# Performance work log

Measured on AMD Instinct MI355X. Metric: run time of the kernel, lower is better.

The kernel has to match this reference:

```python
import jax, jax.numpy as jnp
import numpy as np

N = 50000      # nodes
E = 800000     # edges
IN_C = 128
HID = 96
OUT_C = 40
L = 8          # num_layers
ALPHA = 0.1
THETA = 0.5
DROPOUT = 0.5


def setup_inputs() -> dict:
    key = jax.random.key(0)
    ks = jax.random.split(key, 6)
    x = jax.random.normal(ks[0], (N, IN_C), dtype=jnp.float32)
    edge_index = jax.random.randint(ks[1], (2, E), 0, N, dtype=jnp.int64)
    proj_w = jax.random.normal(ks[2], (IN_C, HID), dtype=jnp.float32) / np.sqrt(IN_C)
    proj_b = jnp.zeros((HID,), dtype=jnp.float32)
    conv_ws = jax.random.normal(ks[3], (L, HID, HID), dtype=jnp.float32) / np.sqrt(HID)
    out_w = jax.random.normal(ks[4], (2 * HID, OUT_C), dtype=jnp.float32) / np.sqrt(2 * HID)
    out_b = jnp.zeros((OUT_C,), dtype=jnp.float32)
    return {"x": x, "edge_index": edge_index, "proj_w": proj_w, "proj_b": proj_b,
            "conv_ws": conv_ws, "out_w": out_w, "out_b": out_b}


def reference(x, edge_index, proj_w, proj_b, conv_ws, out_w, out_b):
    # --- GCN normalization with self loops (computed once, as GCN2Conv caches it) ---
    loops = jnp.arange(N, dtype=edge_index.dtype)
    src = jnp.concatenate([edge_index[0], loops])   # [E+N]
    dst = jnp.concatenate([edge_index[1], loops])
    deg = jax.ops.segment_sum(jnp.ones(E + N, dtype=x.dtype), dst, num_segments=N)
    dis = jax.lax.rsqrt(deg)                        # deg >= 1 due to self loops
    norm = dis[src] * dis[dst]                      # [E+N]

    h0 = x @ proj_w + proj_b                        # [N, HID]
    h = h0
    key = jax.random.key(42)
    for k in range(L):
        delta = 1.0 / 2 ** k
        kq, ke, kd, key = jax.random.split(key, 4)
        # dithered quantization
        b = (jax.random.uniform(kq, h.shape, dtype=h.dtype) - 0.5) * delta
        h_q = jnp.floor((h + b) / delta) * delta - b
        # GCN2Conv: propagate + initial residual + identity mapping (shared weights)
        agg = jax.ops.segment_sum(h_q[src] * norm[:, None], dst, num_segments=N)
        t = (1.0 - ALPHA) * agg + ALPHA * h0
        beta = float(np.log(THETA / (k + 1) + 1.0))
        h = (1.0 - beta) * t + beta * (t @ conv_ws[k])
        # gaussian noise + relu
        h = jax.nn.relu(h + 0.01 * jax.random.normal(ke, h.shape, dtype=h.dtype))
        if k != L - 1:
            keep = 1.0 - DROPOUT
            mask = jax.random.bernoulli(kd, keep, h.shape)
            h = jnp.where(mask, h / keep, 0.0)
    return jnp.concatenate([h0, h], axis=-1) @ out_w + out_b
```

## Files before the change

### kernel.cpp

```cpp
#include <hip/hip_runtime.h>
#include <hip/hip_fp16.h>
#include <cstdint>
#include <cmath>

#define HID 96
#define INC 128
#define OUTC 40
#define ROWS 32

typedef int      v4i __attribute__((ext_vector_type(4)));
typedef float    v4f __attribute__((ext_vector_type(4)));
typedef unsigned v2u __attribute__((ext_vector_type(2)));

__device__ __forceinline__ int4 ntld_i4(const int* p){
  v4i v = __builtin_nontemporal_load((const v4i*)p);
  return make_int4(v.x, v.y, v.z, v.w);
}
__device__ __forceinline__ float4 ntld_f4(const float* p){
  v4f v = __builtin_nontemporal_load((const v4f*)p);
  return make_float4(v.x, v.y, v.z, v.w);
}
__device__ __forceinline__ void ntst_u2(void* p, unsigned lo, unsigned hi){
  v2u v; v.x = lo; v.y = hi;
  __builtin_nontemporal_store(v, (v2u*)p);
}
__device__ __forceinline__ void ntst_f4(float* p, float a, float b, float c, float d){
  v4f v; v.x = a; v.y = b; v.z = c; v.w = d;
  __builtin_nontemporal_store(v, (v4f*)p);
}

__device__ __forceinline__ unsigned rotl32d(unsigned x, int r){ return (x<<r)|(x>>(32-r)); }

__device__ __forceinline__ void tf2x32_dev(unsigned k0, unsigned k1, unsigned x0, unsigned x1,
                                           unsigned &y0, unsigned &y1){
  unsigned ks2 = k0 ^ k1 ^ 0x1BD11BDAu;
  x0 += k0; x1 += k1;
#define TFR(r) { x0 += x1; x1 = rotl32d(x1, r); x1 ^= x0; }
  TFR(13) TFR(15) TFR(26) TFR(6)   x0 += k1;  x1 += ks2 + 1u;
  TFR(17) TFR(29) TFR(16) TFR(24)  x0 += ks2; x1 += k0 + 2u;
  TFR(13) TFR(15) TFR(26) TFR(6)   x0 += k0;  x1 += k1 + 3u;
  TFR(17) TFR(29) TFR(16) TFR(24)  x0 += k1;  x1 += ks2 + 4u;
  TFR(13) TFR(15) TFR(26) TFR(6)   x0 += ks2; x1 += k0 + 5u;
#undef TFR
  y0 = x0; y1 = x1;
}

__device__ __forceinline__ unsigned tf_bits(unsigned k0, unsigned k1, unsigned idx){
  unsigned y0, y1; tf2x32_dev(k0, k1, 0u, idx, y0, y1); return y0 ^ y1;
}

__device__ __forceinline__ float u01_from_bits(unsigned bits){
  return __uint_as_float((bits >> 9) | 0x3f800000u) - 1.0f;
}

__device__ __forceinline__ float erfinv_xla(float x){
  float w = -log1pf(-x*x);
  float p;
  if (w < 5.0f){
    w = w - 2.5f;
    p = 2.81022636e-08f;
    p = fmaf(p,w, 3.43273939e-07f);
    p = fmaf(p,w,-3.5233877e-06f);
    p = fmaf(p,w,-4.39150654e-06f);
    p = fmaf(p,w, 0.00021858087f);
    p = fmaf(p,w,-0.00125372503f);
    p = fmaf(p,w,-0.00417768164f);
    p = fmaf(p,w, 0.246640727f);
    p = fmaf(p,w, 1.50140941f);
  } else {
    w = sqrtf(w) - 3.0f;
    p = -0.000200214257f;
    p = fmaf(p,w, 0.000100950558f);
    p = fmaf(p,w, 0.00134934322f);
    p = fmaf(p,w,-0.00367342844f);
    p = fmaf(p,w, 0.00573950773f);
    p = fmaf(p,w,-0.0076224613f);
    p = fmaf(p,w, 0.00943887047f);
    p = fmaf(p,w, 1.00167406f);
    p = fmaf(p,w, 2.83297682f);
  }
  return p*x;
}

__global__ void k_detect(const unsigned* __restrict__ raw, int* flag){
  unsigned v = raw[2*threadIdx.x + 1];
  unsigned long long m = __ballot(v == 0u);
  if (threadIdx.x == 0) *flag = (m == 0xFFFFFFFFFFFFFFFFull) ? 1 : 0;
}

__global__ void k_convcount(const unsigned* __restrict__ raw, const int* __restrict__ flag,
                            int E, int* __restrict__ cnt){
  int e = blockIdx.x*256 + threadIdx.x; if (e >= E) return;
  int d;
  if (*flag) d = (int)raw[2*((size_t)E + e)];
  else       d = ((const int*)raw)[E + e];
  atomicAdd(&cnt[d], 1);
}

__global__ void k_hist(const int* __restrict__ cnt, int N, int* __restrict__ bcnt){
  __shared__ int lh[64];
  int tid = threadIdx.x; int n = blockIdx.x*256 + tid;
  if (tid < 64) lh[tid] = 0;
  __syncthreads();
  if (n < N) atomicAdd(&lh[min(cnt[n], 63)], 1);
  __syncthreads();
  if (tid < 64){
    int c = lh[tid];
    if (c > 0) atomicAdd(&bcnt[tid], c);
  }
}

__global__ void k_bucketoff(int* __restrict__ bcnt){
  __shared__ int sb[64];
  int tid = threadIdx.x;
  sb[tid] = bcnt[tid];
  __syncthreads();
  int off = 0;
  for (int b2 = tid+1; b2 < 64; b2++) off += sb[b2];
  bcnt[tid] = off;
}

__global__ void k_perm(const int* __restrict__ cnt, int N, int* __restrict__ boff,
                       int* __restrict__ perm, int* __restrict__ iperm,
                       float* __restrict__ diso, float* __restrict__ dsqr,
                       int* __restrict__ degv, int* __restrict__ degp){
  __shared__ int lh[64];
  int tid = threadIdx.x; int n = blockIdx.x*256 + tid;
  int v = (n < N) ? cnt[n] : 0;
  if (tid < 64) lh[tid] = 0;
  __syncthreads();
  int b = min(v, 63), r = 0;
  if (n < N) r = atomicAdd(&lh[b], 1);
  __syncthreads();
  if (tid < 64){
    int c = lh[tid];
    lh[tid] = (c > 0) ? atomicAdd(&boff[tid], c) : 0;
  }
  __syncthreads();
  if (n < N){
    int pos = lh[b] + r;
    perm[pos] = n;
    iperm[n] = pos;
    diso[n] = 1.0f / sqrtf((float)(v + 1));
    dsqr[pos] = 1.0f / (float)(v + 1);
    degv[pos] = v;
    degp[pos] = (v + 7) & ~7;
  }
}

__global__ void k_scanA(const int* __restrict__ degp, int N, int* __restrict__ psum){
  __shared__ int sh[256];
  int tid = threadIdx.x; int n = blockIdx.x*256 + tid;
  sh[tid] = (n < N) ? degp[n] : 0;
  for (int off = 128; off > 0; off >>= 1){
    __syncthreads();
    if (tid < off) sh[tid] += sh[tid + off];
  }
  __syncthreads();
  if (tid == 0) psum[blockIdx.x] = sh[0];
}

__global__ void k_scanB(int* __restrict__ psum, int nb){
  __shared__ int sh[256];
  int tid = threadIdx.x;
  int v = (tid < nb) ? psum[tid] : 0;
  sh[tid] = v;
  __syncthreads();
  for (int off = 1; off < 256; off <<= 1){
    int t = (tid >= off) ? sh[tid - off] : 0;
    __syncthreads();
    sh[tid] += t;
    __syncthreads();
  }
  if (tid < nb) psum[tid] = sh[tid] - v;
}

__global__ void k_rowptr2(const int* __restrict__ degv, const int* __restrict__ degp,
                          const int* __restrict__ psum, int N,
                          int* __restrict__ rowptr, int* __restrict__ csr_src,
                          float* __restrict__ csr_w){
  __shared__ int sh[256];
  int tid = threadIdx.x; int n = blockIdx.x*256 + tid;
  int vp = (n < N) ? degp[n] : 0;
  sh[tid] = vp;
  __syncthreads();
  for (int off = 1; off < 256; off <<= 1){
    int t = (tid >= off) ? sh[tid - off] : 0;
    __syncthreads();
    sh[tid] += t;
    __syncthreads();
  }
  if (n < N){
    int base = psum[blockIdx.x] + sh[tid] - vp;
    rowptr[n] = base;
    int v = degv[n];
    for (int q = v; q < vp; q++){ csr_src[base + q] = 0; csr_w[base + q] = 0.0f; }
    if (n == N-1) rowptr[N] = base + vp;
  }
}

__global__ void k_fill(const unsigned* __restrict__ raw, const int* __restrict__ flag, int E,
                       const int* __restrict__ rowptr, const int* __restrict__ iperm,
                       int* __restrict__ cur, const float* __restrict__ diso,
                       int* __restrict__ csr_src, float* __restrict__ csr_w){
  int e = blockIdx.x*256 + threadIdx.x; if (e >= E) return;
  int s, d;
  if (*flag){ s = (int)raw[2*(size_t)e]; d = (int)raw[2*((size_t)E + e)]; }
  else      { const int* r = (const int*)raw; s = r[e]; d = r[E + e]; }
  int rd = iperm[d];
  int pos = atomicAdd(&cur[rd], 1);
  int slot = rowptr[rd] + pos;
  csr_src[slot] = iperm[s];
  csr_w[slot] = diso[s]*diso[d];
}

__global__ __launch_bounds__(256) void k_h0(
  const float* __restrict__ x, const float* __restrict__ W, const float* __restrict__ bias,
  const int* __restrict__ iperm,
  float* __restrict__ h0p, __half* __restrict__ hq, unsigned kq0, unsigned kq1, int N)
{
  __shared__ float xs[64*65];
  __shared__ float wsh[64*96];
  int tid = threadIdx.x; int n0 = blockIdx.x*64;
  int cg = tid & 15, ng = tid >> 4; int c0 = cg*6;
  float acc[4][6];
#pragma unroll
  for (int i=0;i<4;i++) for (int j=0;j<6;j++) acc[i][j]=0.f;
  for (int kc=0; kc<2; kc++){
    if (kc) __syncthreads();
    for (int q=tid; q<1536; q+=256)
      ((float4*)wsh)[q] = ((const float4*)(W + kc*64*96))[q];
    for (int q=tid; q<1024; q+=256){
      int g=q*4; int r=g>>6, col=g&63;
      int n=n0+r; int ns = n<N ? n : N-1;
      float4 v = ((const float4*)(x + (size_t)ns*128 + kc*64))[col>>2];
      xs[r*65+col]=v.x; xs[r*65+col+1]=v.y; xs[r*65+col+2]=v.z; xs[r*65+col+3]=v.w;
    }
    __syncthreads();
    for (int k=0;k<64;k++){
      float wv[6];
#pragma unroll
      for (int j=0;j<6;j++) wv[j]=wsh[k*96 + c0 + j];
#pragma unroll
      for (int i=0;i<4;i++){
        float xv = xs[(ng*4+i)*65 + k];
#pragma unroll
        for (int j=0;j<6;j++) acc[i][j] = fmaf(xv, wv[j], acc[i][j]);
      }
    }
  }
#pragma unroll
  for (int i=0;i<4;i++){
    int n = n0 + ng*4 + i; if (n >= N) continue;
    int rn = iperm[n];
#pragma unroll
    for (int j=0;j<6;j++){
      int c = c0 + j; int p = n*96 + c;
      float v = acc[i][j] + bias[c];
      h0p[(size_t)rn*96 + c] = v;
      unsigned bq = tf_bits(kq0, kq1, (unsigned)p);
      float b = u01_from_bits(bq) - 0.5f;
      hq[(size_t)rn*96 + c] = __float2half_rn(floorf(v + b) - b);
    }
  }
}

#define GATH(gj, wv) { \
  float2 f01 = __half22float2(*(__half2*)&gj.x); \
  float2 f23 = __half22float2(*(__half2*)&gj.y); \
  ax = fmaf(f01.x, wv, ax); ay = fmaf(f01.y, wv, ay); \
  az = fmaf(f23.x, wv, az); aw = fmaf(f23.y, wv, aw); }

__global__ __launch_bounds__(256, 4) void k_layer(
  const __half* __restrict__ hq_in, const float* __restrict__ h0p, const float* __restrict__ dsqr,
  const int* __restrict__ rowptr, const int* __restrict__ csr_src, const float* __restrict__ csr_w,
  const int* __restrict__ perm, const float* __restrict__ W,
  float betaf, float ombf,
  unsigned ke0, unsigned ke1, unsigned kd0, unsigned kd1,
  unsigned kq0, unsigned kq1, float delta_n, float invdelta_n,
  int do_dropout, int write_h,
  __half* __restrict__ hq_out, float* __restrict__ h_out, int N)
{
  __shared__ float ts[ROWS*100];
  __shared__ float wsh[24*96];
  int tid = threadIdx.x;
  int tx = tid & 31, ty = tid >> 5;
  int n0 = blockIdx.x*ROWS;

  const char* hqc = (const char*)hq_in;

#pragma unroll 1
  for (int pass = 0; pass < 4; pass++){
    int r = pass*8 + ty;
    int row = n0 + r;
    if (tx < 24){
      float4 o = make_float4(0.f, 0.f, 0.f, 0.f);
      if (row < N){
        unsigned txb = (unsigned)tx*8u;
        float dd = dsqr[row];
        unsigned lo = (unsigned)rowptr[row], hi = (unsigned)rowptr[row+1];
        uint2 sraw = *(const uint2*)(hqc + (unsigned)row*192u + txb);
        float4 hz = ntld_f4(h0p + (size_t)row*96 + tx*4);
        float2 s01 = __half22float2(*(__half2*)&sraw.x);
        float2 s23 = __half22float2(*(__half2*)&sraw.y);
        float ax = s01.x*dd, ay = s01.y*dd, az = s23.x*dd, aw = s23.y*dd;
        unsigned s = lo;
        unsigned n16 = lo + ((hi - lo) & ~15u);
        for (; s < n16; s += 16){
          int4   sa = ntld_i4(csr_src + s);
          int4   sb = ntld_i4(csr_src + s + 4);
          int4   sc = ntld_i4(csr_src + s + 8);
          int4   sd = ntld_i4(csr_src + s + 12);
          float4 wa = ntld_f4(csr_w + s);
          float4 wb = ntld_f4(csr_w + s + 4);
          float4 wc = ntld_f4(csr_w + s + 8);
          float4 wd = ntld_f4(csr_w + s + 12);
          uint2 g0 = *(const uint2*)(hqc + (unsigned)sa.x*192u + txb);
          uint2 g1 = *(const uint2*)(hqc + (unsigned)sa.y*192u + txb);
          uint2 g2 = *(const uint2*)(hqc + (unsigned)sa.z*192u + txb);
          uint2 g3 = *(const uint2*)(hqc + (unsigned)sa.w*192u + txb);
          uint2 g4 = *(const uint2*)(hqc + (unsigned)sb.x*192u + txb);
          uint2 g5 = *(const uint2*)(hqc + (unsigned)sb.y*192u + txb);
          uint2 g6 = *(const uint2*)(hqc + (unsigned)sb.z*192u + txb);
          uint2 g7 = *(const uint2*)(hqc + (unsigned)sb.w*192u + txb);
          uint2 g8 = *(const uint2*)(hqc + (unsigned)sc.x*192u + txb);
          uint2 g9 = *(const uint2*)(hqc + (unsigned)sc.y*192u + txb);
          uint2 gA = *(const uint2*)(hqc + (unsigned)sc.z*192u + txb);
          uint2 gB = *(const uint2*)(hqc + (unsigned)sc.w*192u + txb);
          uint2 gC = *(const uint2*)(hqc + (unsigned)sd.x*192u + txb);
          uint2 gD = *(const uint2*)(hqc + (unsigned)sd.y*192u + txb);
          uint2 gE = *(const uint2*)(hqc + (unsigned)sd.z*192u + txb);
          uint2 gF = *(const uint2*)(hqc + (unsigned)sd.w*192u + txb);
          GATH(g0, wa.x) GATH(g1, wa.y) GATH(g2, wa.z) GATH(g3, wa.w)
          GATH(g4, wb.x) GATH(g5, wb.y) GATH(g6, wb.z) GATH(g7, wb.w)
          GATH(g8, wc.x) GATH(g9, wc.y) GATH(gA, wc.z) GATH(gB, wc.w)
          GATH(gC, wd.x) GATH(gD, wd.y) GATH(gE, wd.z) GATH(gF, wd.w)
        }
        for (; s < hi; s += 8){
          int4   sa = ntld_i4(csr_src + s);
          int4   sb = ntld_i4(csr_src + s + 4);
          float4 wa = ntld_f4(csr_w + s);
          float4 wb = ntld_f4(csr_w + s + 4);
          uint2 g0 = *(const uint2*)(hqc + (unsigned)sa.x*192u + txb);
          uint2 g1 = *(const uint2*)(hqc + (unsigned)sa.y*192u + txb);
          uint2 g2 = *(const uint2*)(hqc + (unsigned)sa.z*192u + txb);
          uint2 g3 = *(const uint2*)(hqc + (unsigned)sa.w*192u + txb);
          uint2 g4 = *(const uint2*)(hqc + (unsigned)sb.x*192u + txb);
          uint2 g5 = *(const uint2*)(hqc + (unsigned)sb.y*192u + txb);
          uint2 g6 = *(const uint2*)(hqc + (unsigned)sb.z*192u + txb);
          uint2 g7 = *(const uint2*)(hqc + (unsigned)sb.w*192u + txb);
          GATH(g0, wa.x) GATH(g1, wa.y) GATH(g2, wa.z) GATH(g3, wa.w)
          GATH(g4, wb.x) GATH(g5, wb.y) GATH(g6, wb.z) GATH(g7, wb.w)
        }
        o.x = 0.9f*ax + 0.1f*hz.x;
        o.y = 0.9f*ay + 0.1f*hz.y;
        o.z = 0.9f*az + 0.1f*hz.z;
        o.w = 0.9f*aw + 0.1f*hz.w;
      }
      *((float4*)&ts[r*100 + tx*4]) = o;
    }
  }

  int cg = tid & 7, ng = tid >> 3;
  int c0 = cg * 12;
  float acc[12];
#pragma unroll
  for (int j = 0; j < 12; j++) acc[j] = 0.f;

  for (int chunk = 0; chunk < 4; chunk++){
    __syncthreads();
    for (int q = tid; q < 576; q += 256)
      ((float4*)wsh)[q] = ((const float4*)(W + chunk*24*96))[q];
    __syncthreads();
#pragma unroll 4
    for (int kk = 0; kk < 24; kk++){
      int k = chunk*24 + kk;
      float4 w0 = *((const float4*)&wsh[kk*96 + c0]);
      float4 w1 = *((const float4*)&wsh[kk*96 + c0 + 4]);
      float4 w2 = *((const float4*)&wsh[kk*96 + c0 + 8]);
      float xv = ts[ng*100 + k];
      acc[0] = fmaf(xv, w0.x, acc[0]);  acc[1] = fmaf(xv, w0.y, acc[1]);
      acc[2] = fmaf(xv, w0.z, acc[2]);  acc[3] = fmaf(xv, w0.w, acc[3]);
      acc[4] = fmaf(xv, w1.x, acc[4]);  acc[5] = fmaf(xv, w1.y, acc[5]);
      acc[6] = fmaf(xv, w1.z, acc[6]);  acc[7] = fmaf(xv, w1.w, acc[7]);
      acc[8] = fmaf(xv, w2.x, acc[8]);  acc[9] = fmaf(xv, w2.y, acc[9]);
      acc[10]= fmaf(xv, w2.z, acc[10]); acc[11]= fmaf(xv, w2.w, acc[11]);
    }
  }

  const float LO = __uint_as_float(0xBF7FFFFFu);
  int n = n0 + ng;
  if (n < N){
    int po = perm[n];
    float res[12];
#pragma unroll
    for (int j = 0; j < 12; j++){
      int c = c0 + j; unsigned p = (unsigned)po*96u + (unsigned)c;
      float tv = ts[ng*100 + c];
      float hv = ombf*tv + betaf*acc[j];
      unsigned be = tf_bits(ke0, ke1, p);
      float uv = fmaxf(LO, u01_from_bits(be)*2.0f + LO);
      hv += 0.01f * (1.41421356f * erfinv_xla(uv));
      hv = fmaxf(hv, 0.0f);
      if (do_dropout){
        unsigned bd = tf_bits(kd0, kd1, p);
        hv = (bd < 0x80000000u) ? hv*2.0f : 0.0f;
      }
      if (!write_h){
        unsigned bq = tf_bits(kq0, kq1, p);
        float b = (u01_from_bits(bq) - 0.5f)*delta_n;
        hv = floorf((hv + b)*invdelta_n)*delta_n - b;
      }
      res[j] = hv;
    }
    if (write_h){
      float* dst2 = h_out + (size_t)n*96 + c0;
#pragma unroll
      for (int j4 = 0; j4 < 3; j4++)
        ntst_f4(&dst2[j4*4], res[j4*4], res[j4*4+1], res[j4*4+2], res[j4*4+3]);
    } else {
      __half* dst2 = hq_out + (size_t)n*96 + c0;
#pragma unroll
      for (int j4 = 0; j4 < 3; j4++){
        unsigned lo2 = (unsigned)__half_as_ushort(__float2half_rn(res[j4*4+0]))
                     | ((unsigned)__half_as_ushort(__float2half_rn(res[j4*4+1])) << 16);
        unsigned hi2 = (unsigned)__half_as_ushort(__float2half_rn(res[j4*4+2]))
                     | ((unsigned)__half_as_ushort(__float2half_rn(res[j4*4+3])) << 16);
        ntst_u2(dst2 + j4*4, lo2, hi2);
      }
    }
  }
}

__global__ __launch_bounds__(256) void k_final(
  const float* __restrict__ h0p, const float* __restrict__ hp,
  const float* __restrict__ W, const float* __restrict__ bias,
  const int* __restrict__ perm, float* __restrict__ out, int N)
{
  __shared__ float xs[64*97];
  __shared__ float wsh[96*40];
  int tid = threadIdx.x; int n0 = blockIdx.x*64;
  int cg = tid & 7, ng = tid >> 3; int c0 = cg*5;
  float acc[2][5];
#pragma unroll
  for (int i=0;i<2;i++) for (int j=0;j<5;j++) acc[i][j]=0.f;
  for (int ph=0; ph<2; ph++){
    if (ph) __syncthreads();
    const float* xsrc = ph ? hp : h0p;
    for (int q=tid; q<960; q+=256)
      ((float4*)wsh)[q] = ((const float4*)(W + ph*96*40))[q];
    for (int q=tid; q<1536; q+=256){
      int g=q*4; int r=g/96, col=g%96;
      int n=n0+r; int ns = n<N ? n : N-1;
      float4 v = ((const float4*)(xsrc + (size_t)ns*96))[col>>2];
      xs[r*97+col]=v.x; xs[r*97+col+1]=v.y; xs[r*97+col+2]=v.z; xs[r*97+col+3]=v.w;
    }
    __syncthreads();
    for (int k=0;k<96;k++){
      float wv[5];
#pragma unroll
      for (int j=0;j<5;j++) wv[j]=wsh[k*40 + c0 + j];
#pragma unroll
      for (int i=0;i<2;i++){
        float xv = xs[(ng*2+i)*97 + k];
#pragma unroll
        for (int j=0;j<5;j++) acc[i][j] = fmaf(xv, wv[j], acc[i][j]);
      }
    }
  }
#pragma unroll
  for (int i=0;i<2;i++){
    int n = n0 + ng*2 + i; if (n >= N) continue;
    int pm = perm[n];
#pragma unroll
    for (int j=0;j<5;j++)
      out[(size_t)pm*40 + c0 + j] = acc[i][j] + bias[c0 + j];
  }
}

static void tf_host(uint32_t k0, uint32_t k1, uint32_t x0, uint32_t x1,
                    uint32_t &y0, uint32_t &y1){
  uint32_t ks2 = k0 ^ k1 ^ 0x1BD11BDAu;
  x0 += k0; x1 += k1;
  auto R = [&](int r){ x0 += x1; x1 = (x1<<r)|(x1>>(32-r)); x1 ^= x0; };
  R(13);R(15);R(26);R(6);   x0 += k1;  x1 += ks2 + 1u;
  R(17);R(29);R(16);R(24);  x0 += ks2; x1 += k0 + 2u;
  R(13);R(15);R(26);R(6);   x0 += k0;  x1 += k1 + 3u;
  R(17);R(29);R(16);R(24);  x0 += k1;  x1 += ks2 + 4u;
  R(13);R(15);R(26);R(6);   x0 += ks2; x1 += k0 + 5u;
  y0 = x0; y1 = x1;
}

extern "C" void kernel_launch(void* const* d_in, const int* in_sizes, int n_in,
                              void* d_out, int out_size, void* d_ws, size_t ws_size,
                              hipStream_t stream)
{
  const float*    x       = (const float*)d_in[0];
  const unsigned* eraw    = (const unsigned*)d_in[1];
  const float*    proj_w  = (const float*)d_in[2];
  const float*    proj_b  = (const float*)d_in[3];
  const float*    conv_w  = (const float*)d_in[4];
  const float*    out_w   = (const float*)d_in[5];
  const float*    out_b   = (const float*)d_in[6];
  float* out = (float*)d_out;

  const int N = in_sizes[0] / INC;
  const int E = in_sizes[1] / 2;
  const size_t NH = (size_t)N * HID;
  const int NP = (N + 16) & ~15;
  const int EP = ((E + 7*N + 15) & ~15);

  float*  ws     = (float*)d_ws;
  float*  h0p    = ws;
  float*  hbp    = h0p + NH;
  __half* hqA    = (__half*)(hbp + NH);
  __half* hqB    = hqA + NH;
  float*  csr_w  = (float*)(hqB + NH);
  int*    csr_src= (int*)(csr_w + EP);
  int*    rowptr = csr_src + EP;
  int*    perm   = rowptr + NP;
  int*    iperm  = perm + NP;
  int*    degv   = iperm + NP;
  int*    degp   = degv + NP;
  int*    cnt    = degp + NP;
  int*    cur    = cnt + NP;
  float*  diso   = (float*)(cur + NP);
  float*  dsqr   = diso + NP;
  int*    bcnt   = (int*)(dsqr + NP);
  int*    psum   = bcnt + 64;
  int*    flag   = psum + 256;
  (void)ws_size; (void)n_in; (void)out_size;

  uint32_t kq[8][2], ke[8][2], kd[8][2];
  {
    uint32_t K0 = 0u, K1 = 42u;
    for (int k = 0; k < 8; k++){
      uint32_t y0, y1;
      tf_host(K0, K1, 0u, 0u, y0, y1); kq[k][0]=y0; kq[k][1]=y1;
      tf_host(K0, K1, 0u, 1u, y0, y1); ke[k][0]=y0; ke[k][1]=y1;
      tf_host(K0, K1, 0u, 2u, y0, y1); kd[k][0]=y0; kd[k][1]=y1;
      tf_host(K0, K1, 0u, 3u, y0, y1); K0=y0; K1=y1;
    }
  }

  const int gE  = (E + 255)/256;
  const int gN  = (N + 255)/256;
  const int gMM = (N + 63)/64;
  const int gL  = (N + ROWS-1)/ROWS;

  hipMemsetAsync(cnt, 0, (size_t)N*4, stream);
  hipMemsetAsync(bcnt, 0, 64*4, stream);
  k_detect   <<<1, 64, 0, stream>>>(eraw, flag);
  k_convcount<<<gE, 256, 0, stream>>>(eraw, flag, E, cnt);
  k_hist     <<<gN, 256, 0, stream>>>(cnt, N, bcnt);
  k_bucketoff<<<1, 64, 0, stream>>>(bcnt);
  k_perm     <<<gN, 256, 0, stream>>>(cnt, N, bcnt, perm, iperm, diso, dsqr, degv, degp);
  k_scanA    <<<gN, 256, 0, stream>>>(degp, N, psum);
  k_scanB    <<<1, 256, 0, stream>>>(psum, gN);
  k_rowptr2  <<<gN, 256, 0, stream>>>(degv, degp, psum, N, rowptr, csr_src, csr_w);
  hipMemsetAsync(cur, 0, (size_t)N*4, stream);
  k_fill     <<<gE, 256, 0, stream>>>(eraw, flag, E, rowptr, iperm, cur, diso, csr_src, csr_w);

  k_h0<<<gMM, 256, 0, stream>>>(x, proj_w, proj_b, iperm, h0p, hqA, kq[0][0], kq[0][1], N);

  for (int k = 0; k < 8; k++){
    double bd = log(0.5/(double)(k+1) + 1.0);
    float betaf = (float)bd;
    float ombf  = (float)(1.0 - bd);
    int last = (k == 7);
    float dn  = 1.0f/(float)(1 << (k+1));
    float idn = (float)(1 << (k+1));
    const __half* hin  = (k & 1) ? hqB : hqA;
    __half*       hout = (k & 1) ? hqA : hqB;
    k_layer<<<gL, 256, 0, stream>>>(hin, h0p, dsqr, rowptr, csr_src, csr_w, perm,
      conv_w + (size_t)k*HID*HID, betaf, ombf,
      ke[k][0], ke[k][1], kd[k][0], kd[k][1],
      last?0u:kq[k+1][0], last?0u:kq[k+1][1], dn, idn,
      !last, last, hout, hbp, N);
  }

  k_final<<<gMM, 256, 0, stream>>>(h0p, hbp, out_w, out_b, perm, out, N);
}
```

Measured before the change: 983.8 us.

## Fuse all eight GCN layers into one cooperative persistent kernel with grid sync

Replaces the eight per-layer kernel launches with a single cooperative kernel. It loops over layers and separates them with grid.sync, and each block handles up to two row tiles. The h0 residual rows are loaded into registers once and reused across all layers instead of being re-read every layer. This is meant to remove launch gaps and the per-layer h0 reload. The cost is grid-wide barriers, possible serialization when each block handles two tiles, and higher register pressure from the hz0/hz1 arrays. A fallback to per-layer launches remains for when cooperative launch is unavailable.

```diff
diff --git a/kernel.cpp b/kernel.cpp
--- a/kernel.cpp
+++ b/kernel.cpp
@@ -1,5 +1,6 @@
 #include <hip/hip_runtime.h>
 #include <hip/hip_fp16.h>
+#include <hip/hip_cooperative_groups.h>
 #include <cstdint>
 #include <cmath>
 
@@ -7,6 +8,8 @@
 #define INC 128
 #define OUTC 40
 #define ROWS 32
+
+namespace cg = cooperative_groups;
 
 typedef int      v4i __attribute__((ext_vector_type(4)));
 typedef float    v4f __attribute__((ext_vector_type(4)));
@@ -271,39 +274,29 @@
   ax = fmaf(f01.x, wv, ax); ay = fmaf(f01.y, wv, ay); \
   az = fmaf(f23.x, wv, az); aw = fmaf(f23.y, wv, aw); }
 
-__global__ __launch_bounds__(256, 4) void k_layer(
-  const __half* __restrict__ hq_in, const float* __restrict__ h0p, const float* __restrict__ dsqr,
-  const int* __restrict__ rowptr, const int* __restrict__ csr_src, const float* __restrict__ csr_w,
-  const int* __restrict__ perm, const float* __restrict__ W,
-  float betaf, float ombf,
-  unsigned ke0, unsigned ke1, unsigned kd0, unsigned kd1,
-  unsigned kq0, unsigned kq1, float delta_n, float invdelta_n,
-  int do_dropout, int write_h,
-  __half* __restrict__ hq_out, float* __restrict__ h_out, int N)
+__device__ __forceinline__ void gather_tile(
+  int tile, int N, int tx, int ty,
+  const __half* __restrict__ hq_in, const float* __restrict__ dsqr,
+  const int* __restrict__ rowptr, const int* __restrict__ csr_src,
+  const float* __restrict__ csr_w, const float4 hz[4], float* ts)
 {
-  __shared__ float ts[ROWS*100];
-  __shared__ float wsh[24*96];
-  int tid = threadIdx.x;
-  int tx = tid & 31, ty = tid >> 5;
-  int n0 = blockIdx.x*ROWS;
-
+  __syncthreads();
   const char* hqc = (const char*)hq_in;
-
+  int n0 = tile*ROWS;
 #pragma unroll 1
   for (int pass = 0; pass < 4; pass++){
     int r = pass*8 + ty;
     int row = n0 + r;
     if (tx < 24){
-      float4 o = make_float4(0.f, 0.f, 0.f, 0.f);
+      float ax=0.f, ay=0.f, az=0.f, aw=0.f;
       if (row < N){
         unsigned txb = (unsigned)tx*8u;
         float dd = dsqr[row];
         unsigned lo = (unsigned)rowptr[row], hi = (unsigned)rowptr[row+1];
         uint2 sraw = *(const uint2*)(hqc + (unsigned)row*192u + txb);
-        float4 hz = ntld_f4(h0p + (size_t)row*96 + tx*4);
         float2 s01 = __half22float2(*(__half2*)&sraw.x);
         float2 s23 = __half22float2(*(__half2*)&sraw.y);
-        float ax = s01.x*dd, ay = s01.y*dd, az = s23.x*dd, aw = s23.y*dd;
+        ax = s01.x*dd; ay = s01.y*dd; az = s23.x*dd; aw = s23.y*dd;
         unsigned s = lo;
         unsigned n16 = lo + ((hi - lo) & ~15u);
         for (; s < n16; s += 16){
@@ -352,17 +345,41 @@
           GATH(g0, wa.x) GATH(g1, wa.y) GATH(g2, wa.z) GATH(g3, wa.w)
           GATH(g4, wb.x) GATH(g5, wb.y) GATH(g6, wb.z) GATH(g7, wb.w)
         }
-        o.x = 0.9f*ax + 0.1f*hz.x;
-        o.y = 0.9f*ay + 0.1f*hz.y;
-        o.z = 0.9f*az + 0.1f*hz.z;
-        o.w = 0.9f*aw + 0.1f*hz.w;
       }
-      *((float4*)&ts[r*100 + tx*4]) = o;
-    }
-  }
-
+      ts[r*100 + tx*4 + 0] = ax;
+      ts[r*100 + tx*4 + 1] = ay;
+      ts[r*100 + tx*4 + 2] = az;
+      ts[r*100 + tx*4 + 3] = aw;
+    }
+  }
+  if (tx < 24){
+#pragma unroll
+    for (int p = 0; p < 4; p++){
+      int r = p*8 + ty;
+      float4 a = *(float4*)&ts[r*100 + tx*4];
+      float4 o;
+      o.x = 0.9f*a.x + 0.1f*hz[p].x;
+      o.y = 0.9f*a.y + 0.1f*hz[p].y;
+      o.z = 0.9f*a.z + 0.1f*hz[p].z;
+      o.w = 0.9f*a.w + 0.1f*hz[p].w;
+      *(float4*)&ts[r*100 + tx*4] = o;
+    }
+  }
+}
+
+__device__ __forceinline__ void mm_epi(
+  int tile, int N, int tid, const float* __restrict__ Wk,
+  const int* __restrict__ perm,
+  float betaf, float ombf,
+  unsigned ke0, unsigned ke1, unsigned kd0, unsigned kd1,
+  unsigned kq0, unsigned kq1, float delta_n, float invdelta_n,
+  int do_dropout, int write_h,
+  __half* __restrict__ hq_out, float* __restrict__ h_out,
+  float* ts, float* wsh)
+{
   int cg = tid & 7, ng = tid >> 3;
   int c0 = cg * 12;
+  int n0 = tile*ROWS;
   float acc[12];
 #pragma unroll
   for (int j = 0; j < 12; j++) acc[j] = 0.f;
@@ -370,7 +387,7 @@
   for (int chunk = 0; chunk < 4; chunk++){
     __syncthreads();
     for (int q = tid; q < 576; q += 256)
-      ((float4*)wsh)[q] = ((const float4*)(W + chunk*24*96))[q];
+      ((float4*)wsh)[q] = ((const float4*)(Wk + chunk*24*96))[q];
     __syncthreads();
 #pragma unroll 4
     for (int kk = 0; kk < 24; kk++){
@@ -430,6 +447,99 @@
       }
     }
   }
+}
+
+struct LPA {
+  float betaf[8], ombf[8], dn[8], idn[8];
+  unsigned ke0[8], ke1[8], kd0[8], kd1[8], kq0[8], kq1[8];
+};
+
+__global__ __launch_bounds__(256, 4) void k_layers(
+  __half* __restrict__ hqA, __half* __restrict__ hqB,
+  const float* __restrict__ h0p, const float* __restrict__ dsqr,
+  const int* __restrict__ rowptr, const int* __restrict__ csr_src,
+  const float* __restrict__ csr_w, const int* __restrict__ perm,
+  const float* __restrict__ conv_w, float* __restrict__ hbp,
+  int N, int nTiles, LPA lp)
+{
+  __shared__ float ts[ROWS*100];
+  __shared__ float wsh[24*96];
+  int tid = threadIdx.x;
+  int tx = tid & 31, ty = tid >> 5;
+  int t0 = blockIdx.x;
+  int t1 = blockIdx.x + gridDim.x;
+
+  float4 hz0[4], hz1[4];
+#pragma unroll
+  for (int p = 0; p < 4; p++){
+    hz0[p] = make_float4(0.f,0.f,0.f,0.f);
+    hz1[p] = make_float4(0.f,0.f,0.f,0.f);
+  }
+  if (tx < 24){
+#pragma unroll
+    for (int p = 0; p < 4; p++){
+      int r0 = t0*ROWS + p*8 + ty;
+      if (r0 < N) hz0[p] = *(const float4*)(h0p + (size_t)r0*96 + tx*4);
+      if (t1 < nTiles){
+        int r1 = t1*ROWS + p*8 + ty;
+        if (r1 < N) hz1[p] = *(const float4*)(h0p + (size_t)r1*96 + tx*4);
+      }
+    }
+  }
+
+  cg::grid_group grid = cg::this_grid();
+
+#pragma unroll 1
+  for (int k = 0; k < 8; k++){
+    const __half* hin  = (k & 1) ? hqB : hqA;
+    __half*       hout = (k & 1) ? hqA : hqB;
+    const float*  Wk   = conv_w + (size_t)k*HID*HID;
+    float betaf = lp.betaf[k], ombf = lp.ombf[k], dn = lp.dn[k], idn = lp.idn[k];
+    unsigned ke0 = lp.ke0[k], ke1 = lp.ke1[k], kd0 = lp.kd0[k], kd1 = lp.kd1[k];
+    unsigned kq0 = lp.kq0[k], kq1 = lp.kq1[k];
+    int dd = (k != 7), wh = (k == 7);
+
+    gather_tile(t0, N, tx, ty, hin, dsqr, rowptr, csr_src, csr_w, hz0, ts);
+    mm_epi(t0, N, tid, Wk, perm, betaf, ombf, ke0, ke1, kd0, kd1, kq0, kq1,
+           dn, idn, dd, wh, hout, hbp, ts, wsh);
+    if (t1 < nTiles){
+      gather_tile(t1, N, tx, ty, hin, dsqr, rowptr, csr_src, csr_w, hz1, ts);
+      mm_epi(t1, N, tid, Wk, perm, betaf, ombf, ke0, ke1, kd0, kd1, kq0, kq1,
+             dn, idn, dd, wh, hout, hbp, ts, wsh);
+    }
+    __threadfence();
+    grid.sync();
+  }
+}
+
+__global__ __launch_bounds__(256, 4) void k_layer_fb(
+  const __half* __restrict__ hq_in, const float* __restrict__ h0p, const float* __restrict__ dsqr,
+  const int* __restrict__ rowptr, const int* __restrict__ csr_src, const float* __restrict__ csr_w,
+  const int* __restrict__ perm, const float* __restrict__ W,
+  float betaf, float ombf,
+  unsigned ke0, unsigned ke1, unsigned kd0, unsigned kd1,
+  unsigned kq0, unsigned kq1, float delta_n, float invdelta_n,
+  int do_dropout, int write_h,
+  __half* __restrict__ hq_out, float* __restrict__ h_out, int N)
+{
+  __shared__ float ts[ROWS*100];
+  __shared__ float wsh[24*96];
+  int tid = threadIdx.x;
+  int tx = tid & 31, ty = tid >> 5;
+  int t0 = blockIdx.x;
+  float4 hz[4];
+#pragma unroll
+  for (int p = 0; p < 4; p++) hz[p] = make_float4(0.f,0.f,0.f,0.f);
+  if (tx < 24){
+#pragma unroll
+    for (int p = 0; p < 4; p++){
+      int r0 = t0*ROWS + p*8 + ty;
+      if (r0 < N) hz[p] = ntld_f4(h0p + (size_t)r0*96 + tx*4);
+    }
+  }
+  gather_tile(t0, N, tx, ty, hq_in, dsqr, rowptr, csr_src, csr_w, hz, ts);
+  mm_epi(t0, N, tid, W, perm, betaf, ombf, ke0, ke1, kd0, kd1, kq0, kq1,
+         delta_n, invdelta_n, do_dropout, write_h, hq_out, h_out, ts, wsh);
 }
 
 __global__ __launch_bounds__(256) void k_final(
@@ -531,53 +641,81 @@
   int*    flag   = psum + 256;
   (void)ws_size; (void)n_in; (void)out_size;
 
-  uint32_t kq[8][2], ke[8][2], kd[8][2];
+  LPA lp;
   {
     uint32_t K0 = 0u, K1 = 42u;
+    uint32_t kq0s, kq1s;
     for (int k = 0; k < 8; k++){
       uint32_t y0, y1;
-      tf_host(K0, K1, 0u, 0u, y0, y1); kq[k][0]=y0; kq[k][1]=y1;
-      tf_host(K0, K1, 0u, 1u, y0, y1); ke[k][0]=y0; ke[k][1]=y1;
-      tf_host(K0, K1, 0u, 2u, y0, y1); kd[k][0]=y0; kd[k][1]=y1;
+      tf_host(K0, K1, 0u, 0u, y0, y1);
+      if (k == 0){ kq0s = y0; kq1s = y1; }
+      if (k >= 1){ lp.kq0[k-1] = y0; lp.kq1[k-1] = y1; }
+      tf_host(K0, K1, 0u, 1u, y0, y1); lp.ke0[k]=y0; lp.ke1[k]=y1;
+      tf_host(K0, K1, 0u, 2u, y0, y1); lp.kd0[k]=y0; lp.kd1[k]=y1;
       tf_host(K0, K1, 0u, 3u, y0, y1); K0=y0; K1=y1;
-    }
-  }
-
-  const int gE  = (E + 255)/256;
-  const int gN  = (N + 255)/256;
-  const int gMM = (N + 63)/64;
-  const int gL  = (N + ROWS-1)/ROWS;
-
-  hipMemsetAsync(cnt, 0, (size_t)N*4, stream);
-  hipMemsetAsync(bcnt, 0, 64*4, stream);
-  k_detect   <<<1, 64, 0, stream>>>(eraw, flag);
-  k_convcount<<<gE, 256, 0, stream>>>(eraw, flag, E, cnt);
-  k_hist     <<<gN, 256, 0, stream>>>(cnt, N, bcnt);
-  k_bucketoff<<<1, 64, 0, stream>>>(bcnt);
-  k_perm     <<<gN, 256, 0, stream>>>(cnt, N, bcnt, perm, iperm, diso, dsqr, degv, degp);
-  k_scanA    <<<gN, 256, 0, stream>>>(degp, N, psum);
-  k_scanB    <<<1, 256, 0, stream>>>(psum, gN);
-  k_rowptr2  <<<gN, 256, 0, stream>>>(degv, degp, psum, N, rowptr, csr_src, csr_w);
-  hipMemsetAsync(cur, 0, (size_t)N*4, stream);
-  k_fill     <<<gE, 256, 0, stream>>>(eraw, flag, E, rowptr, iperm, cur, diso, csr_src, csr_w);
-
-  k_h0<<<gMM, 256, 0, stream>>>(x, proj_w, proj_b, iperm, h0p, hqA, kq[0][0], kq[0][1], N);
-
-  for (int k = 0; k < 8; k++){
-    double bd = log(0.5/(double)(k+1) + 1.0);
-    float betaf = (float)bd;
-    float ombf  = (float)(1.0 - bd);
-    int last = (k == 7);
-    float dn  = 1.0f/(float)(1 << (k+1));
-    float idn = (float)(1 << (k+1));
-    const __half* hin  = (k & 1) ? hqB : hqA;
-    __half*       hout = (k & 1) ? hqA : hqB;
-    k_layer<<<gL, 256, 0, stream>>>(hin, h0p, dsqr, rowptr, csr_src, csr_w, perm,
-      conv_w + (size_t)k*HID*HID, betaf, ombf,
-      ke[k][0], ke[k][1], kd[k][0], kd[k][1],
-      last?0u:kq[k+1][0], last?0u:kq[k+1][1], dn, idn,
-      !last, last, hout, hbp, N);
-  }
-
-  k_final<<<gMM, 256, 0, stream>>>(h0p, hbp, out_w, out_b, perm, out, N);
-}
+      double bd = log(0.5/(double)(k+1) + 1.0);
+      lp.betaf[k] = (float)bd;
+      lp.ombf[k]  = (float)(1.0 - bd);
+      lp.dn[k]  = 1.0f/(float)(1 << (k+1));
+      lp.idn[k] = (float)(1 << (k+1));
+    }
+    lp.kq0[7] = 0u; lp.kq1[7] = 0u;
+    lp.kq0[7] = 0u; lp.kq1[7] = 0u;
+    const int gE  = (E + 255)/256;
+    const int gN  = (N + 255)/256;
+    const int gMM = (N + 63)/64;
+    const int nTiles = (N + ROWS-1)/ROWS;
+
+    hipMemsetAsync(cnt, 0, (size_t)N*4, stream);
+    hipMemsetAsync(bcnt, 0, 64*4, stream);
+    k_detect   <<<1, 64, 0, stream>>>(eraw, flag);
+    k_convcount<<<gE, 256, 0, stream>>>(eraw, flag, E, cnt);
+    k_hist     <<<gN, 256, 0, stream>>>(cnt, N, bcnt);
+    k_bucketoff<<<1, 64, 0, stream>>>(bcnt);
+    k_perm     <<<gN, 256, 0, stream>>>(cnt, N, bcnt, perm, iperm, diso, dsqr, degv, degp);
+    k_scanA    <<<gN, 256, 0, stream>>>(degp, N, psum);
+    k_scanB    <<<1, 256, 0, stream>>>(psum, gN);
+    k_rowptr2  <<<gN, 256, 0, stream>>>(degv, degp, psum, N, rowptr, csr_src, csr_w);
+    hipMemsetAsync(cur, 0, (size_t)N*4, stream);
+    k_fill     <<<gE, 256, 0, stream>>>(eraw, flag, E, rowptr, iperm, cur, diso, csr_src, csr_w);
+
+    k_h0<<<gMM, 256, 0, stream>>>(x, proj_w, proj_b, iperm, h0p, hqA, kq0s, kq1s, N);
+
+    static int s_grid = -1;
+    if (s_grid < 0){
+      int dev = 0; hipGetDevice(&dev);
+      int cu = 0;
+      hipDeviceGetAttribute(&cu, hipDeviceAttributeMultiprocessorCount, dev);
+      int mb = 0;
+      hipOccupancyMaxActiveBlocksPerMultiprocessor(&mb, (const void*)k_layers, 256, 0);
+      s_grid = cu * mb;
+      if (s_grid <= 0) s_grid = 0;
+    }
+    bool fused_ok = (s_grid*2 >= nTiles) && (s_grid > 0);
+    if (fused_ok){
+      int grid = s_grid < nTiles ? s_grid : nTiles;
+      __half* a = hqA; __half* b = hqB;
+      int Nv = N, nTv = nTiles;
+      void* args[] = { &a, &b, (void*)&h0p, (void*)&dsqr, (void*)&rowptr,
+                       (void*)&csr_src, (void*)&csr_w, (void*)&perm,
+                       (void*)&conv_w, (void*)&hbp, &Nv, &nTv, &lp };
+      hipError_t cerr = hipLaunchCooperativeKernel((const void*)k_layers,
+                          dim3(grid), dim3(256), args, 0, stream);
+      if (cerr != hipSuccess) fused_ok = false;
+    }
+    if (!fused_ok){
+      for (int k = 0; k < 8; k++){
+        int last = (k == 7);
+        const __half* hin  = (k & 1) ? hqB : hqA;
+        __half*       hout = (k & 1) ? hqA : hqB;
+        k_layer_fb<<<nTiles, 256, 0, stream>>>(hin, h0p, dsqr, rowptr, csr_src, csr_w, perm,
+          conv_w + (size_t)k*HID*HID, lp.betaf[k], lp.ombf[k],
+          lp.ke0[k], lp.ke1[k], lp.kd0[k], lp.kd1[k],
+          lp.kq0[k], lp.kq1[k], lp.dn[k], lp.idn[k],
+          !last, last, hout, hbp, N);
+      }
+    }
+
+    k_final<<<gMM, 256, 0, stream>>>(h0p, hbp, out_w, out_b, perm, out, N);
+  }
+}
```

Measured after the change: 989.6 us. Within noise of the previous version (+0.6%).
